# Performance work log

Measured on AMD Instinct MI355X. Metric: run time of the kernel, lower is better.

Reference implementation:

```python
import jax, jax.numpy as jnp
import numpy as np

T, D, N, K, H = 2048, 4096, 32, 8, 128
ROPE_THETA = 500000.0


def setup_inputs() -> dict:
    key = jax.random.key(0)
    ks = jax.random.split(key, 5)
    s = 0.02
    return {
        "x": jax.random.normal(ks[0], (T, D), jnp.float32) * s,
        "positions": jnp.arange(T, dtype=jnp.int64 if jax.config.jax_enable_x64 else jnp.int32),
        "Wq": jax.random.normal(ks[1], (D, N, H), jnp.float32) * s,
        "Wk": jax.random.normal(ks[2], (D, K, H), jnp.float32) * s,
        "Wv": jax.random.normal(ks[3], (D, K, H), jnp.float32) * s,
        "Wo": jax.random.normal(ks[4], (N, H, D), jnp.float32) * s,
    }


def _rope(positions, q, k):
    # positions: [T]; q: [T,N,H]; k: [T,K,H]. Half-split rotation (Llama style).
    half = H // 2
    inv_freq = 1.0 / (ROPE_THETA ** (jnp.arange(0, half, dtype=jnp.float32) / half))
    ang = positions.astype(jnp.float32)[:, None] * inv_freq  # [T, H/2]
    cos = jnp.cos(ang)[:, None, :]  # [T,1,H/2]
    sin = jnp.sin(ang)[:, None, :]

    def rot(x):
        x1, x2 = x[..., :half], x[..., half:]
        return jnp.concatenate([x1 * cos - x2 * sin, x2 * cos + x1 * sin], axis=-1)

    return rot(q), rot(k)


def reference(x, positions, Wq, Wk, Wv, Wo):
    q = jnp.einsum('td,dnh->tnh', x, Wq)  # [T,N,H]
    k = jnp.einsum('td,dkh->tkh', x, Wk)  # [T,K,H]
    v = jnp.einsum('td,dkh->tkh', x, Wv)
    q, k = _rope(positions, q, k)

    rep = N // K  # GQA: expand kv heads to query heads
    kr = jnp.repeat(k, rep, axis=1)  # [T,N,H]
    vr = jnp.repeat(v, rep, axis=1)

    scale = 1.0 / jnp.sqrt(jnp.asarray(H, jnp.float32))
    scores = jnp.einsum('tnh,snh->nts', q, kr) * scale  # [N,T,T]
    causal = positions[:, None] >= positions[None, :]   # [T,T]
    scores = jnp.where(causal[None, :, :], scores, jnp.finfo(scores.dtype).min)
    probs = jax.nn.softmax(scores, axis=-1)
    ctx = jnp.einsum('nts,snh->tnh', probs, vr)  # [T,N,H]
    return jnp.einsum('tnh,nhd->td', ctx, Wo)
```

## Files before the change

### kernel.cpp

```cpp
#include <hip/hip_runtime.h>
#include <hip/hip_bf16.h>

#define T_SEQ 2048
#define D_MODEL 4096
#define N_HEADS 32
#define K_HEADS 8
#define HEAD_DIM 128

typedef unsigned short u16;
typedef short sfrag8 __attribute__((ext_vector_type(8)));
typedef float ffrag4 __attribute__((ext_vector_type(4)));

#if defined(__has_builtin)
#  if __has_builtin(__builtin_amdgcn_exp2f)
#    define EXP2F(x) __builtin_amdgcn_exp2f(x)
#  else
#    define EXP2F(x) exp2f(x)
#  endif
#else
#  define EXP2F(x) exp2f(x)
#endif

#define QSCALE_LOG2E 0.12751744900463627f
#define NEG_L2_THETA_64 (-0.29580575889569f)

__device__ __forceinline__ float bf2f(u16 u) {
    return __uint_as_float(((unsigned int)u) << 16);
}
__device__ __forceinline__ u16 f2bf(float f) {
    unsigned int x = __float_as_uint(f);
    unsigned int r = (x + 0x7fffu + ((x >> 16) & 1u)) >> 16;
    return (u16)r;
}
__device__ __forceinline__ uint4 pack8(const float4 a, const float4 b) {
    uint4 r;
    r.x = (unsigned)f2bf(a.x) | ((unsigned)f2bf(a.y) << 16);
    r.y = (unsigned)f2bf(a.z) | ((unsigned)f2bf(a.w) << 16);
    r.z = (unsigned)f2bf(b.x) | ((unsigned)f2bf(b.y) << 16);
    r.w = (unsigned)f2bf(b.z) | ((unsigned)f2bf(b.w) << 16);
    return r;
}

__device__ __forceinline__ void gload_lds16(const u16* g, u16* l) {
    __builtin_amdgcn_global_load_lds(
        (const __attribute__((address_space(1))) void*)g,
        (__attribute__((address_space(3))) void*)l, 16, 0, 0);
}

__global__ __launch_bounds__(256) void convert_bf16(
    const float* __restrict__ X, u16* __restrict__ Y, int n8)
{
    const int i = blockIdx.x * 256 + threadIdx.x;
    if (i < n8) {
        float4 a = ((const float4*)X)[(size_t)i * 2];
        float4 b = ((const float4*)X)[(size_t)i * 2 + 1];
        ((uint4*)Y)[i] = pack8(a, b);
    }
}

__global__ __launch_bounds__(256) void transpose_f32_bf16(
    const float* __restrict__ W, u16* __restrict__ WT, int R, int C)
{
    __shared__ float Ts[64][65];
    const int t = threadIdx.x;
    const int c0 = blockIdx.x * 64, r0 = blockIdx.y * 64;
    const int rl = t >> 4, cl = (t & 15) * 4;
#pragma unroll
    for (int p = 0; p < 4; ++p) {
        const int r = p * 16 + rl;
        float4 v = *(const float4*)(W + (size_t)(r0 + r) * C + c0 + cl);
        Ts[r][cl] = v.x; Ts[r][cl + 1] = v.y; Ts[r][cl + 2] = v.z; Ts[r][cl + 3] = v.w;
    }
    __syncthreads();
    const int nl = t >> 2, k4 = (t & 3) * 16;
    u16 tmp[16];
#pragma unroll
    for (int j = 0; j < 16; ++j) tmp[j] = f2bf(Ts[k4 + j][nl]);
    u16* dst = WT + (size_t)(c0 + nl) * R + r0 + k4;
    *(uint4*)(dst) = *(uint4*)&tmp[0];
    *(uint4*)(dst + 8) = *(uint4*)&tmp[8];
}

template <int CMODE>
__global__ __launch_bounds__(256) void gemm_bt(
    const u16* __restrict__ A, const u16* __restrict__ BT,
    void* __restrict__ Cp, int M, int Nb, int Kd, int ldc)
{
    __shared__ __align__(16) u16 SmemAll[2 * 128 * 64];
    u16* As = SmemAll;
    u16* Bs = SmemAll + 128 * 64;

    const int tid = threadIdx.x;
    const int lane = tid & 63;
    const int w = tid >> 6;
    const int wm = w >> 1, wn = w & 1;
    const int ln = lane & 15, quad = lane >> 4;

    int wid = blockIdx.y * gridDim.x + blockIdx.x;
    const int nwg = gridDim.x * gridDim.y;
    const int cpx = nwg >> 3;
    wid = (wid & 7) * cpx + (wid >> 3);
    const int bx = wid % gridDim.x;
    const int by = wid / gridDim.x;

    const int m0 = by * 128, n0 = bx * 128;

    size_t aoff[4], boff[4];
#pragma unroll
    for (int i = 0; i < 4; ++i) {
        const int row = (i * 4 + w) * 8 + (lane >> 3);
        const int cg = (lane & 7) ^ (lane >> 3);
        aoff[i] = (size_t)(m0 + row) * Kd + cg * 8;
        boff[i] = (size_t)(n0 + row) * Kd + cg * 8;
    }

    ffrag4 acc[4][4];
#pragma unroll
    for (int mi = 0; mi < 4; ++mi)
#pragma unroll
        for (int ni = 0; ni < 4; ++ni) acc[mi][ni] = (ffrag4){0.f, 0.f, 0.f, 0.f};

    for (int k0 = 0; k0 < Kd; k0 += 64) {
#pragma unroll
        for (int i = 0; i < 4; ++i) {
            gload_lds16(A + aoff[i] + k0, &As[(i * 4 + w) * 512]);
            gload_lds16(BT + boff[i] + k0, &Bs[(i * 4 + w) * 512]);
        }
        __syncthreads();

#pragma unroll
        for (int kk = 0; kk < 2; ++kk) {
            sfrag8 af[4], bfv[4];
#pragma unroll
            for (int mi = 0; mi < 4; ++mi) {
                const int row = wm * 64 + mi * 16 + ln;
                const int pc = ((kk * 4) | quad) ^ (ln & 7);
                af[mi] = *(const sfrag8*)&As[row * 64 + pc * 8];
            }
#pragma unroll
            for (int ni = 0; ni < 4; ++ni) {
                const int row = wn * 64 + ni * 16 + ln;
                const int pc = ((kk * 4) | quad) ^ (ln & 7);
                bfv[ni] = *(const sfrag8*)&Bs[row * 64 + pc * 8];
            }
#pragma unroll
            for (int mi = 0; mi < 4; ++mi)
#pragma unroll
                for (int ni = 0; ni < 4; ++ni)
                    acc[mi][ni] = __builtin_amdgcn_mfma_f32_16x16x32_bf16(
                        af[mi], bfv[ni], acc[mi][ni], 0, 0, 0);
        }
        __syncthreads();
    }

    if constexpr (CMODE == 4) {
        u16* base = (u16*)Cp;
        if (n0 < 5120) {
#pragma unroll
            for (int mi = 0; mi < 4; ++mi)
#pragma unroll
                for (int ni = 0; ni < 4; ++ni) {
                    const int colL = wn * 64 + ni * 16 + ln;
#pragma unroll
                    for (int i = 0; i < 4; ++i) {
                        const int rowL = wm * 64 + mi * 16 + quad * 4 + i;
                        SmemAll[rowL * 128 + colL] = f2bf(acc[mi][ni][i]);
                    }
                }
            __syncthreads();
            float invf[4];
#pragma unroll
            for (int ni = 0; ni < 4; ++ni)
                invf[ni] = EXP2F((float)(ni * 16 + ln) * NEG_L2_THETA_64);
#pragma unroll
            for (int mi = 0; mi < 4; ++mi)
#pragma unroll
                for (int ni = 0; ni < 4; ++ni) {
                    const int colL = wn * 64 + ni * 16 + ln;
                    const int fi = colL & 63;
                    const int gcol = n0 + colL;
#pragma unroll
                    for (int i = 0; i < 4; ++i) {
                        const int rowL = wm * 64 + mi * 16 + quad * 4 + i;
                        const int grow = m0 + rowL;
                        const float x1 = bf2f(SmemAll[rowL * 128 + fi]);
                        const float x2 = bf2f(SmemAll[rowL * 128 + fi + 64]);
                        const float ang = (float)grow * invf[ni];
                        const float cw = cosf(ang);
                        const float sw = sinf(ang);
                        const float o = (wn == 0) ? (x1 * cw - x2 * sw)
                                                  : (x2 * cw + x1 * sw);
                        const u16 v = f2bf(o);
                        if (gcol < 4096) {
                            base[4194304u + (size_t)grow * 4096 + gcol] = v;
                        } else {
                            base[(size_t)grow * 1024 + (gcol - 4096)] = v;
                        }
                    }
                }
        } else {
#pragma unroll
            for (int mi = 0; mi < 4; ++mi)
#pragma unroll
                for (int ni = 0; ni < 4; ++ni) {
                    const int gcol = n0 + wn * 64 + ni * 16 + ln;
#pragma unroll
                    for (int i = 0; i < 4; ++i) {
                        const int grow = m0 + wm * 64 + mi * 16 + quad * 4 + i;
                        base[2097152u + (size_t)(gcol - 5120) * T_SEQ + grow] =
                            f2bf(acc[mi][ni][i]);
                    }
                }
        }
        return;
    }

#pragma unroll
    for (int mi = 0; mi < 4; ++mi) {
#pragma unroll
        for (int ni = 0; ni < 4; ++ni) {
            const int gcol = n0 + wn * 64 + ni * 16 + ln;
#pragma unroll
            for (int i = 0; i < 4; ++i) {
                const int grow = m0 + wm * 64 + mi * 16 + quad * 4 + i;
                if constexpr (CMODE == 1) {
                    ((float*)Cp)[(size_t)grow * ldc + gcol] = acc[mi][ni][i];
                } else {
                    ((u16*)Cp)[(size_t)grow * ldc + gcol] = f2bf(acc[mi][ni][i]);
                }
            }
        }
    }
}

template <int AMODE, int CMODE>
__global__ __launch_bounds__(256) void gemm_any(
    const void* __restrict__ Ap, const float* __restrict__ B, void* __restrict__ Cp,
    int M, int Nb, int Kd, int ldc)
{
    __shared__ __align__(16) u16 As[64 * 64];
    __shared__ __align__(16) u16 Bs[64 * 72];

    const int tid = threadIdx.x;
    const int n0 = blockIdx.x * 64, m0 = blockIdx.y * 64;

    const int lr = tid >> 3;
    const int cc8 = tid & 7;
    const int sw = ((cc8 ^ (lr & 7)) * 8);
    const int dstA0 = lr * 64 + sw;
    const int dstA1 = (lr + 32) * 64 + sw;
    const size_t arow0 = (size_t)(m0 + lr) * Kd;
    const size_t arow1 = (size_t)(m0 + lr + 32) * Kd;

    const int kr = tid >> 2;
    const int ncb = (tid & 3) * 16;

    const int lane = tid & 63;
    const int w = tid >> 6;
    const int col16 = lane & 15;
    const int quad = lane >> 4;
    const int swl = lane & 7;
    const int mrow = w * 16 + col16;

    ffrag4 acc[4];
#pragma unroll
    for (int j = 0; j < 4; ++j) acc[j] = (ffrag4){0.f, 0.f, 0.f, 0.f};

    for (int k0 = 0; k0 < Kd; k0 += 64) {
        if constexpr (AMODE == 1) {
            const u16* Af = (const u16*)Ap;
            uint4 va0 = *(const uint4*)(Af + arow0 + k0 + cc8 * 8);
            uint4 va1 = *(const uint4*)(Af + arow1 + k0 + cc8 * 8);
            *(uint4*)&As[dstA0] = va0;
            *(uint4*)&As[dstA1] = va1;
        } else {
            const float* Af = (const float*)Ap;
            float4 a00 = *(const float4*)(Af + arow0 + k0 + cc8 * 8);
            float4 a01 = *(const float4*)(Af + arow0 + k0 + cc8 * 8 + 4);
            float4 a10 = *(const float4*)(Af + arow1 + k0 + cc8 * 8);
            float4 a11 = *(const float4*)(Af + arow1 + k0 + cc8 * 8 + 4);
            *(uint4*)&As[dstA0] = pack8(a00, a01);
            *(uint4*)&As[dstA1] = pack8(a10, a11);
        }
        {
            const float* bp = B + (size_t)(k0 + kr) * Nb + n0 + ncb;
            float4 b0 = *(const float4*)(bp);
            float4 b1 = *(const float4*)(bp + 4);
            float4 b2 = *(const float4*)(bp + 8);
            float4 b3 = *(const float4*)(bp + 12);
            u16 tmp[16];
            tmp[0] = f2bf(b0.x); tmp[1] = f2bf(b0.y); tmp[2] = f2bf(b0.z); tmp[3] = f2bf(b0.w);
            tmp[4] = f2bf(b1.x); tmp[5] = f2bf(b1.y); tmp[6] = f2bf(b1.z); tmp[7] = f2bf(b1.w);
            tmp[8] = f2bf(b2.x); tmp[9] = f2bf(b2.y); tmp[10] = f2bf(b2.z); tmp[11] = f2bf(b2.w);
            tmp[12] = f2bf(b3.x); tmp[13] = f2bf(b3.y); tmp[14] = f2bf(b3.z); tmp[15] = f2bf(b3.w);
#pragma unroll
            for (int e = 0; e < 16; ++e)
                Bs[(ncb + e) * 72 + kr] = tmp[e];
        }
        __syncthreads();
#pragma unroll
        for (int c = 0; c < 2; ++c) {
            const int cc = c * 4 + quad;
            const int koffA = (cc ^ swl) * 8;
            sfrag8 af = *(const sfrag8*)&As[mrow * 64 + koffA];
#pragma unroll
            for (int j = 0; j < 4; ++j) {
                sfrag8 bfv = *(const sfrag8*)&Bs[(j * 16 + col16) * 72 + cc * 8];
                acc[j] = __builtin_amdgcn_mfma_f32_16x16x32_bf16(af, bfv, acc[j], 0, 0, 0);
            }
        }
        __syncthreads();
    }

#pragma unroll
    for (int j = 0; j < 4; ++j) {
        const int gcol = n0 + j * 16 + col16;
#pragma unroll
        for (int i = 0; i < 4; ++i) {
            const int grow = m0 + w * 16 + quad * 4 + i;
            if constexpr (CMODE == 1) {
                ((float*)Cp)[(size_t)grow * ldc + gcol] = acc[j][i];
            } else if constexpr (CMODE == 2) {
                ((u16*)Cp)[(size_t)gcol * ldc + grow] = f2bf(acc[j][i]);
            } else {
                ((u16*)Cp)[(size_t)grow * ldc + gcol] = f2bf(acc[j][i]);
            }
        }
    }
}

__global__ __launch_bounds__(64) void rope_kernel(
    u16* __restrict__ buf, int nheads, int t0)
{
    const int h = blockIdx.x;
    const int t = blockIdx.y;
    u16* rowp = buf + ((size_t)t * nheads + h) * HEAD_DIM;
    const int i = threadIdx.x;
    const float p = (float)(t0 + t);
    const float inv = expf(-((float)i * (1.0f / 64.0f)) * 13.122363377404329f);
    const float ang = p * inv;
    const float c = cosf(ang);
    const float s = sinf(ang);
    const float x1 = bf2f(rowp[i]);
    const float x2 = bf2f(rowp[i + 64]);
    rowp[i] = f2bf(x1 * c - x2 * s);
    rowp[i + 64] = f2bf(x2 * c + x1 * s);
}

__global__ __launch_bounds__(256) void attn_mfma(
    const u16* q, const u16* __restrict__ k,
    const u16* __restrict__ vt, u16* ctx, int t0)
{
    __shared__ __align__(16) u16 Kt[64 * 136];
    __shared__ __align__(16) u16 Vt[128 * 72];
    __shared__ __align__(16) u16 Ps[4][16 * 72];

    const int head = blockIdx.x;
    const int qt = gridDim.y - 1 - blockIdx.y;
    const int kvh = head >> 2;
    const int tid = threadIdx.x;
    const int lane = tid & 63;
    const int w = tid >> 6;
    const int ln = lane & 15;
    const int quad = lane >> 4;

    const int kr = tid >> 2;
    const int c4 = (tid & 3) * 32;
    const int vd = tid >> 1;
    const int vh = (tid & 1) * 32;

    const int qrow_loc = qt * 64 + w * 16 + ln;
    sfrag8 qf[4];
    {
        const u16* qg = q + ((size_t)qrow_loc * N_HEADS + head) * HEAD_DIM;
#pragma unroll
        for (int kk = 0; kk < 4; ++kk)
            qf[kk] = *(const sfrag8*)(qg + kk * 32 + quad * 8);
    }

    ffrag4 acc_o[8];
#pragma unroll
    for (int dt = 0; dt < 8; ++dt) acc_o[dt] = (ffrag4){0.f, 0.f, 0.f, 0.f};
    float mrow[4] = {-INFINITY, -INFINITY, -INFINITY, -INFINITY};
    float lrow_l[4] = {0.f, 0.f, 0.f, 0.f};

    const int Tq0 = t0 + qt * 64;
    const int nst = Tq0 / 64 + 1;
    const int qabs_base = Tq0 + w * 16 + quad * 4;

    for (int st = 0; st < nst; ++st) {
        const int kv0 = st * 64;
        const bool diag = (st == nst - 1);

        __syncthreads();
        {
            const u16* kg = k + ((size_t)(kv0 + kr) * K_HEADS + kvh) * HEAD_DIM + c4;
            u16* kd = &Kt[kr * 136 + c4];
#pragma unroll
            for (int j = 0; j < 4; ++j)
                *(uint4*)(kd + j * 8) = *(const uint4*)(kg + j * 8);
        }
        {
            const u16* vg = vt + ((size_t)(kvh * 128 + vd)) * T_SEQ + kv0 + vh;
            u16* vdst = &Vt[vd * 72 + vh];
#pragma unroll
            for (int j = 0; j < 4; ++j)
                *(uint4*)(vdst + j * 8) = *(const uint4*)(vg + j * 8);
        }
        __syncthreads();

        const int ktc = diag ? ((w < 2) ? 2 : 4) : 4;
        ffrag4 sacc[4];
        __builtin_amdgcn_s_setprio(1);
#pragma unroll
        for (int kt = 0; kt < 4; ++kt) {
            if (kt >= ktc) break;
            sacc[kt] = (ffrag4){0.f, 0.f, 0.f, 0.f};
#pragma unroll
            for (int kk = 0; kk < 4; ++kk) {
                sfrag8 bfr = *(const sfrag8*)&Kt[(kt * 16 + ln) * 136 + kk * 32 + quad * 8];
                sacc[kt] = __builtin_amdgcn_mfma_f32_16x16x32_bf16(qf[kk], bfr, sacc[kt], 0, 0, 0);
            }
        }
        __builtin_amdgcn_s_setprio(0);
        float sv[4][4];
#pragma unroll
        for (int kt = 0; kt < 4; ++kt) {
            if (kt >= ktc) break;
            const int key_abs = kv0 + kt * 16 + ln;
#pragma unroll
            for (int i = 0; i < 4; ++i) {
                float s = sacc[kt][i] * QSCALE_LOG2E;
                if (diag && key_abs > qabs_base + i) s = -INFINITY;
                sv[kt][i] = s;
            }
        }
        bool grew = false;
#pragma unroll
        for (int kt = 0; kt < 4; ++kt) {
            if (kt >= ktc) break;
#pragma unroll
            for (int i = 0; i < 4; ++i)
                grew |= (sv[kt][i] > mrow[i] + 8.0f);
        }
        if (__any(grew)) {
            float tm[4];
#pragma unroll
            for (int i = 0; i < 4; ++i) {
                float t = sv[0][i];
                for (int kt = 1; kt < ktc; ++kt) t = fmaxf(t, sv[kt][i]);
                t = fmaxf(t, __shfl_xor(t, 1));
                t = fmaxf(t, __shfl_xor(t, 2));
                t = fmaxf(t, __shfl_xor(t, 4));
                t = fmaxf(t, __shfl_xor(t, 8));
                tm[i] = t;
            }
            float alpha[4];
#pragma unroll
            for (int i = 0; i < 4; ++i) {
                const float mn = fmaxf(mrow[i], tm[i]);
                alpha[i] = EXP2F(mrow[i] - mn);
                mrow[i] = mn;
            }
            const bool noop = (alpha[0] == 1.f) && (alpha[1] == 1.f) &&
                              (alpha[2] == 1.f) && (alpha[3] == 1.f);
            if (!__all(noop)) {
#pragma unroll
                for (int i = 0; i < 4; ++i) {
                    lrow_l[i] *= alpha[i];
#pragma unroll
                    for (int dt = 0; dt < 8; ++dt) acc_o[dt][i] *= alpha[i];
                }
            }
        }
#pragma unroll
        for (int kt = 0; kt < 4; ++kt) {
            if (kt >= ktc) break;
#pragma unroll
            for (int i = 0; i < 4; ++i) {
                const float p = EXP2F(sv[kt][i] - mrow[i]);
                lrow_l[i] += p;
                Ps[w][(quad * 4 + i) * 72 + kt * 16 + ln] = f2bf(p);
            }
        }
        const int kbm = ktc >> 1;
        __builtin_amdgcn_s_setprio(1);
#pragma unroll
        for (int kb = 0; kb < 2; ++kb) {
            if (kb >= kbm) break;
            sfrag8 afr = *(const sfrag8*)&Ps[w][ln * 72 + kb * 32 + quad * 8];
#pragma unroll
            for (int dt = 0; dt < 8; ++dt) {
                sfrag8 bfr = *(const sfrag8*)&Vt[(dt * 16 + ln) * 72 + kb * 32 + quad * 8];
                acc_o[dt] = __builtin_amdgcn_mfma_f32_16x16x32_bf16(afr, bfr, acc_o[dt], 0, 0, 0);
            }
        }
        __builtin_amdgcn_s_setprio(0);
    }

    float invl[4];
#pragma unroll
    for (int i = 0; i < 4; ++i) {
        float t = lrow_l[i];
        t += __shfl_xor(t, 1);
        t += __shfl_xor(t, 2);
        t += __shfl_xor(t, 4);
        t += __shfl_xor(t, 8);
        invl[i] = 1.0f / t;
    }
#pragma unroll
    for (int i = 0; i < 4; ++i) {
        u16* og = ctx + ((size_t)(qt * 64 + w * 16 + quad * 4 + i) * N_HEADS + head) * HEAD_DIM;
#pragma unroll
        for (int dt = 0; dt < 8; ++dt)
            og[dt * 16 + ln] = f2bf(acc_o[dt][i] * invl[i]);
    }
}

extern "C" void kernel_launch(void* const* d_in, const int* in_sizes, int n_in,
                              void* d_out, int out_size, void* d_ws, size_t ws_size,
                              hipStream_t stream) {
    (void)in_sizes; (void)n_in; (void)out_size;
    const float* x  = (const float*)d_in[0];
    const float* Wq = (const float*)d_in[2];
    const float* Wk = (const float*)d_in[3];
    const float* Wv = (const float*)d_in[4];
    const float* Wo = (const float*)d_in[5];
    float* out = (float*)d_out;
    char* ws = (char*)d_ws;
    const size_t MiB = 1024 * 1024;

    if (ws_size >= 88 * MiB) {
        u16* kbuf  = (u16*)(ws);
        u16* vtbuf = (u16*)(ws + 4 * MiB);
        u16* qsl   = (u16*)(ws + 8 * MiB);
        u16* xb    = (u16*)(ws + 24 * MiB);
        u16* WqkvT = (u16*)(ws + 40 * MiB);

        convert_bf16<<<dim3(T_SEQ * D_MODEL / 8 / 256), 256, 0, stream>>>(
            x, xb, T_SEQ * D_MODEL / 8);
        transpose_f32_bf16<<<dim3(64, 64), 256, 0, stream>>>(
            Wq, WqkvT, D_MODEL, N_HEADS * HEAD_DIM);
        transpose_f32_bf16<<<dim3(16, 64), 256, 0, stream>>>(
            Wk, WqkvT + (size_t)4096 * 4096, D_MODEL, K_HEADS * HEAD_DIM);
        transpose_f32_bf16<<<dim3(16, 64), 256, 0, stream>>>(
            Wv, WqkvT + (size_t)5120 * 4096, D_MODEL, K_HEADS * HEAD_DIM);

        gemm_bt<4><<<dim3(48, 16), 256, 0, stream>>>(
            xb, WqkvT, ws, T_SEQ, 6144, D_MODEL, 0);

        attn_mfma<<<dim3(N_HEADS, T_SEQ / 64), 256, 0, stream>>>(
            qsl, kbuf, vtbuf, qsl, 0);

        transpose_f32_bf16<<<dim3(64, 64), 256, 0, stream>>>(
            Wo, WqkvT, N_HEADS * HEAD_DIM, D_MODEL);
        gemm_bt<1><<<dim3(32, 16), 256, 0, stream>>>(
            qsl, WqkvT, out, T_SEQ, D_MODEL, N_HEADS * HEAD_DIM, D_MODEL);
        return;
    }

    u16* kbuf  = (u16*)(ws);
    u16* vtbuf = (u16*)(ws + 4194304);
    u16* qsl   = (u16*)(ws + 8388608);

    int S = 8;
    if (ws_size >= (size_t)8388608 + 16777216)      S = 1;
    else if (ws_size >= (size_t)8388608 + 8388608)  S = 2;
    else if (ws_size >= (size_t)8388608 + 4194304)  S = 4;
    const int Ts = T_SEQ / S;

    gemm_any<0, 0><<<dim3(16, T_SEQ / 64), 256, 0, stream>>>(
        x, Wk, kbuf, T_SEQ, K_HEADS * HEAD_DIM, D_MODEL, K_HEADS * HEAD_DIM);
    gemm_any<0, 2><<<dim3(16, T_SEQ / 64), 256, 0, stream>>>(
        x, Wv, vtbuf, T_SEQ, K_HEADS * HEAD_DIM, D_MODEL, T_SEQ);
    rope_kernel<<<dim3(K_HEADS, T_SEQ), 64, 0, stream>>>(kbuf, K_HEADS, 0);

    for (int s = 0; s < S; ++s) {
        const int t0 = s * Ts;
        gemm_any<0, 0><<<dim3(64, Ts / 64), 256, 0, stream>>>(
            x + (size_t)t0 * D_MODEL, Wq, qsl, Ts, D_MODEL, D_MODEL, D_MODEL);
        rope_kernel<<<dim3(N_HEADS, Ts), 64, 0, stream>>>(qsl, N_HEADS, t0);
        attn_mfma<<<dim3(N_HEADS, Ts / 64), 256, 0, stream>>>(
            qsl, kbuf, vtbuf, qsl, t0);
        gemm_any<1, 1><<<dim3(64, Ts / 64), 256, 0, stream>>>(
            qsl, Wo, out + (size_t)t0 * D_MODEL, Ts, D_MODEL, N_HEADS * HEAD_DIM, D_MODEL);
    }
}
```

Baseline: 524.0 us.

## Double-buffer K/V tiles with direct global-to-LDS loads and XOR swizzle

Replaces the synchronous register-staged K and V tile copies with direct global-to-LDS loads into two LDS buffers. The loads for the next KV tile are issued right after the loop-top barrier, so they overlap the current tile's QK and PV MFMA work, and one barrier per iteration is removed. The padded LDS rows are replaced by an XOR-swizzled layout to avoid bank conflicts on fragment reads. This doubles K/V LDS use, which may lower occupancy, and it relies on the barrier to wait for the outstanding LDS-destined loads.

Result: faster. 508.9 us (-2.9%).

```diff
diff --git a/kernel.cpp b/kernel.cpp
--- a/kernel.cpp
+++ b/kernel.cpp
@@ -351,8 +351,8 @@
     const u16* q, const u16* __restrict__ k,
     const u16* __restrict__ vt, u16* ctx, int t0)
 {
-    __shared__ __align__(16) u16 Kt[64 * 136];
-    __shared__ __align__(16) u16 Vt[128 * 72];
+    __shared__ __align__(16) u16 Ktb[2][64 * 128];
+    __shared__ __align__(16) u16 Vtb[2][128 * 64];
     __shared__ __align__(16) u16 Ps[4][16 * 72];
 
     const int head = blockIdx.x;
@@ -364,11 +364,6 @@
     const int ln = lane & 15;
     const int quad = lane >> 4;
 
-    const int kr = tid >> 2;
-    const int c4 = (tid & 3) * 32;
-    const int vd = tid >> 1;
-    const int vh = (tid & 1) * 32;
-
     const int qrow_loc = qt * 64 + w * 16 + ln;
     sfrag8 qf[4];
     {
@@ -378,6 +373,28 @@
             qf[kk] = *(const sfrag8*)(qg + kk * 32 + quad * 8);
     }
 
+    const int krow_l = lane >> 4;
+    const int kcl    = lane & 15;
+    const int vrow_l = lane >> 3;
+    const int vcl    = lane & 7;
+
+    auto stage = [&](int kv0s, int buf) {
+#pragma unroll
+        for (int i = 0; i < 4; ++i) {
+            const int seg = i * 4 + w;
+            const int krow = seg * 4 + krow_l;
+            const int kcg = kcl ^ (krow & 7);
+            gload_lds16(
+                k + ((size_t)(kv0s + krow) * K_HEADS + kvh) * HEAD_DIM + kcg * 8,
+                &Ktb[buf][seg * 512]);
+            const int vrow = seg * 8 + vrow_l;
+            const int vcg = vcl ^ (vrow & 7);
+            gload_lds16(
+                vt + ((size_t)(kvh * 128 + vrow)) * T_SEQ + kv0s + vcg * 8,
+                &Vtb[buf][seg * 512]);
+        }
+    };
+
     ffrag4 acc_o[8];
 #pragma unroll
     for (int dt = 0; dt < 8; ++dt) acc_o[dt] = (ffrag4){0.f, 0.f, 0.f, 0.f};
@@ -388,26 +405,15 @@
     const int nst = Tq0 / 64 + 1;
     const int qabs_base = Tq0 + w * 16 + quad * 4;
 
+    stage(0, 0);
+    int cur = 0;
+
     for (int st = 0; st < nst; ++st) {
         const int kv0 = st * 64;
         const bool diag = (st == nst - 1);
 
         __syncthreads();
-        {
-            const u16* kg = k + ((size_t)(kv0 + kr) * K_HEADS + kvh) * HEAD_DIM + c4;
-            u16* kd = &Kt[kr * 136 + c4];
-#pragma unroll
-            for (int j = 0; j < 4; ++j)
-                *(uint4*)(kd + j * 8) = *(const uint4*)(kg + j * 8);
-        }
-        {
-            const u16* vg = vt + ((size_t)(kvh * 128 + vd)) * T_SEQ + kv0 + vh;
-            u16* vdst = &Vt[vd * 72 + vh];
-#pragma unroll
-            for (int j = 0; j < 4; ++j)
-                *(uint4*)(vdst + j * 8) = *(const uint4*)(vg + j * 8);
-        }
-        __syncthreads();
+        if (st + 1 < nst) stage(kv0 + 64, cur ^ 1);
 
         const int ktc = diag ? ((w < 2) ? 2 : 4) : 4;
         ffrag4 sacc[4];
@@ -418,7 +424,8 @@
             sacc[kt] = (ffrag4){0.f, 0.f, 0.f, 0.f};
 #pragma unroll
             for (int kk = 0; kk < 4; ++kk) {
-                sfrag8 bfr = *(const sfrag8*)&Kt[(kt * 16 + ln) * 136 + kk * 32 + quad * 8];
+                sfrag8 bfr = *(const sfrag8*)&Ktb[cur][
+                    (kt * 16 + ln) * 128 + (((kk * 4 + quad) ^ (ln & 7)) * 8)];
                 sacc[kt] = __builtin_amdgcn_mfma_f32_16x16x32_bf16(qf[kk], bfr, sacc[kt], 0, 0, 0);
             }
         }
@@ -491,11 +498,13 @@
             sfrag8 afr = *(const sfrag8*)&Ps[w][ln * 72 + kb * 32 + quad * 8];
 #pragma unroll
             for (int dt = 0; dt < 8; ++dt) {
-                sfrag8 bfr = *(const sfrag8*)&Vt[(dt * 16 + ln) * 72 + kb * 32 + quad * 8];
+                sfrag8 bfr = *(const sfrag8*)&Vtb[cur][
+                    (dt * 16 + ln) * 64 + (((kb * 4 + quad) ^ (ln & 7)) * 8)];
                 acc_o[dt] = __builtin_amdgcn_mfma_f32_16x16x32_bf16(afr, bfr, acc_o[dt], 0, 0, 0);
             }
         }
         __builtin_amdgcn_s_setprio(0);
+        cur ^= 1;
     }
 
     float invl[4];
```
